# Kernel tuning notes

Measured on AMD Instinct MI355X. Metric: run time of the kernel, lower is better.

## Reference

```python
import jax, jax.numpy as jnp
import numpy as np

B, T, H, K, V, O = 4, 2048, 512, 128, 128, 512


def setup_inputs() -> dict:
    key = jax.random.key(0)
    k0, k1, k2 = jax.random.split(key, 3)
    hidden_state = jax.random.normal(k0, (B, T, H), dtype=jnp.float32)
    cell_state = jnp.zeros((B, K, V), dtype=jnp.float32)
    # fused projection: hidden -> [query K, key K, gate K, value V]
    lim_p = np.sqrt(6.0 / (H + 3 * K + V)).astype(np.float32)  # xavier uniform
    proj_w = jax.random.uniform(k1, (3 * K + V, H), jnp.float32, -lim_p, lim_p)
    proj_b = jnp.zeros((3 * K + V,), jnp.float32)
    lim_o = np.sqrt(6.0 / (2 * V + O)).astype(np.float32)
    out_w = jax.random.uniform(k2, (O, 2 * V), jnp.float32, -lim_o, lim_o)
    out_b = jnp.zeros((O,), jnp.float32)
    return {"hidden_state": hidden_state, "cell_state": cell_state,
            "proj_w": proj_w, "proj_b": proj_b, "out_w": out_w, "out_b": out_b}


def reference(hidden_state, cell_state, proj_w, proj_b, out_w, out_b):
    Bq, Tq, _ = hidden_state.shape
    qkgv = hidden_state @ proj_w.T + proj_b          # (B,T,3K+V)
    query = qkgv[..., :K]
    kgate = jax.nn.sigmoid(qkgv[..., K:2 * K])       # key (sigmoid)
    gate = jax.nn.sigmoid(qkgv[..., 2 * K:3 * K])
    value = jnp.tanh(qkgv[..., 3 * K:])              # (B,T,V)

    def step(C, xs):
        q_t, k_t, g_t, v_t = xs                      # (B,K),(B,K),(B,K),(B,V)
        C = C * g_t[..., None] + k_t[..., None] * v_t[..., None, :]  # (B,K,V)
        o_t = jnp.einsum('bkv,bk->bv', C, q_t)       # C^T q
        return C, o_t

    xs = (query.swapaxes(0, 1), kgate.swapaxes(0, 1),
          gate.swapaxes(0, 1), value.swapaxes(0, 1))
    C_final, ov = jax.lax.scan(step, cell_state, xs)
    ov = ov.swapaxes(0, 1)                           # (B,T,V) output_val per step

    # causal Luong dot attention over the growing bank of past output_vals
    scores = jnp.einsum('btv,bsv->bts', ov, ov)      # (B,T,T)
    causal = jnp.tril(jnp.ones((Tq, Tq), dtype=bool))
    scores = jnp.where(causal, scores, -jnp.inf)
    attn = jax.nn.softmax(scores, axis=-1)
    context = jnp.einsum('bts,bsv->btv', attn, ov)   # (B,T,V)

    outputs = jnp.concatenate([ov, context], axis=-1) @ out_w.T + out_b  # (B,T,O)
    return outputs, C_final
```

## Files before the change

### kernel.cpp

```cpp
#include <hip/hip_runtime.h>
#include <hip/hip_bf16.h>


typedef __attribute__((ext_vector_type(8))) short bf16x8;
typedef __attribute__((ext_vector_type(4))) float f32x4;
typedef __attribute__((ext_vector_type(4))) short short4v;

#define MFMA(a,b,c) __builtin_amdgcn_mfma_f32_16x16x32_bf16(a,b,c,0,0,0)

__device__ __forceinline__ short f2b(float x){
  union { float f; unsigned u; } v; v.f = x;
  unsigned r = v.u + 0x7fffu + ((v.u >> 16) & 1u);
  return (short)(r >> 16);
}
__device__ __forceinline__ float b2f(short h){
  union { unsigned u; float f; } v;
  v.u = ((unsigned)(unsigned short)h) << 16;
  return v.f;
}
__device__ __forceinline__ void split2(float x, short& h, short& l){
  h = f2b(x);
  l = f2b(x - b2f(h));
}
__device__ __forceinline__ void gload16(const void* g, void* l){
  __builtin_amdgcn_global_load_lds(
    (__attribute__((address_space(1))) unsigned int*)(void*)(g),
    (__attribute__((address_space(3))) unsigned int*)(l), 16, 0, 0);
}

__global__ void k_split(const float* __restrict__ in, short* __restrict__ hi,
                        short* __restrict__ lo, int n){
  int i = (blockIdx.x * blockDim.x + threadIdx.x) * 4;
  if (i < n){
    float4 v = *(const float4*)(in + i);
    short4v h, l;
    short th, tl;
    split2(v.x, th, tl); h.x = th; l.x = tl;
    split2(v.y, th, tl); h.y = th; l.y = tl;
    split2(v.z, th, tl); h.z = th; l.z = tl;
    split2(v.w, th, tl); h.w = th; l.w = tl;
    *(short4v*)(hi + i) = h;
    *(short4v*)(lo + i) = l;
  }
}

__global__ void k_cvt(const float* __restrict__ in, short* __restrict__ out, int n){
  int i = (blockIdx.x * blockDim.x + threadIdx.x) * 4;
  if (i < n){
    float4 v = *(const float4*)(in + i);
    short4v o; o.x = f2b(v.x); o.y = f2b(v.y); o.z = f2b(v.z); o.w = f2b(v.w);
    *(short4v*)(out + i) = o;
  }
}

__global__ __launch_bounds__(256) void k_gemm1(
    const short* __restrict__ Ah, const short* __restrict__ Al,
    const short* __restrict__ Bh, const short* __restrict__ Bl,
    const float* __restrict__ bias,
    float* __restrict__ q_o, float* __restrict__ kg_o,
    float* __restrict__ lg_o, float* __restrict__ vv_o)
{
  __shared__ __align__(16) short At[128*64];
  __shared__ __align__(16) short Bt[64*64];
  const int m0 = blockIdx.x * 128;
  const int ny = blockIdx.y;
  const int tid = threadIdx.x, lane = tid & 63;
  const int w = tid >> 6;
  const int wu = __builtin_amdgcn_readfirstlane(w);
  const int wr = w >> 1, wc = w & 1;
  const int coll = lane & 15, rq = lane >> 4;
  f32x4 acc[4][2];
#pragma unroll
  for (int i = 0; i < 4; i++)
#pragma unroll
    for (int j = 0; j < 2; j++) acc[i][j] = (f32x4){0.f,0.f,0.f,0.f};

  for (int step = 0; step < 24; ++step){
    const int seg = step >> 3;
    const int k0 = (step & 7) * 64;
    const short* Asrc = (seg < 2) ? Ah : Al;
    const short* Bsrc = (seg == 1) ? Bl : Bh;
    __syncthreads();
#pragma unroll
    for (int t = 0; t < 4; ++t){
      int ci0 = t*256 + wu*64;
      int ci = ci0 + lane;
      int row = ci >> 3;
      int cs = (ci & 7) ^ (row & 7);
      gload16(Asrc + (size_t)(m0 + row)*512 + k0 + cs*8, At + (size_t)ci0*8);
    }
#pragma unroll
    for (int t = 0; t < 2; ++t){
      int ci0 = t*256 + wu*64;
      int ci = ci0 + lane;
      int row = ci >> 3;
      int cs = (ci & 7) ^ (row & 7);
      gload16(Bsrc + (size_t)(ny*64 + row)*512 + k0 + cs*8, Bt + (size_t)ci0*8);
    }
    __syncthreads();
#pragma unroll
    for (int kk = 0; kk < 2; ++kk){
      bf16x8 a[4], b[2];
#pragma unroll
      for (int mi = 0; mi < 4; mi++){
        int ar = wr*64 + mi*16 + coll;
        a[mi] = *(const bf16x8*)&At[ar*64 + (((kk*4+rq) ^ (ar & 7))*8)];
      }
#pragma unroll
      for (int ni = 0; ni < 2; ni++){
        int br = wc*32 + ni*16 + coll;
        b[ni] = *(const bf16x8*)&Bt[br*64 + (((kk*4+rq) ^ (br & 7))*8)];
      }
#pragma unroll
      for (int mi = 0; mi < 4; mi++)
#pragma unroll
        for (int ni = 0; ni < 2; ni++)
          acc[mi][ni] = MFMA(a[mi], b[ni], acc[mi][ni]);
    }
  }
  const int sec = ny >> 1;
  const int jb  = (ny & 1) * 64;
#pragma unroll
  for (int mi = 0; mi < 4; mi++)
#pragma unroll
  for (int ni = 0; ni < 2; ni++){
    int gl = wc*32 + ni*16 + coll;
    float bsv = bias[ny*64 + gl];
    int jj = jb + gl;
#pragma unroll
    for (int r = 0; r < 4; r++){
      int gm = m0 + wr*64 + mi*16 + rq*4 + r;
      float v = acc[mi][ni][r] + bsv;
      size_t idx = (size_t)gm * 128 + jj;
      if (sec == 0)      q_o[idx] = v;
      else if (sec == 1) kg_o[idx] = 1.f / (1.f + __expf(-v));
      else if (sec == 2) lg_o[idx] = (v > 0.f) ? -log1pf(__expf(-v)) : (v - log1pf(__expf(v)));
      else               vv_o[idx] = tanhf(v);
    }
  }
}

__global__ __launch_bounds__(128) void k_prep(
  const float* __restrict__ q_f, const float* __restrict__ kg_f,
  const float* __restrict__ lg_f, const float* __restrict__ vv_f,
  short* __restrict__ qth, short* __restrict__ qtl,
  short* __restrict__ kth, short* __restrict__ ktl,
  short* __restrict__ khTh, short* __restrict__ khTl,
  short* __restrict__ vvTh, short* __restrict__ vvTl,
  float* __restrict__ Dend)
{
  const int bc = blockIdx.x;
  const int kx = threadIdx.x;
  const size_t base = ((size_t)(bc >> 6) * 2048 + (size_t)(bc & 63) * 32) * 128 + kx;
  double L[32];
  double Lr = 0.0;
#pragma unroll
  for (int s = 0; s < 32; s++){
    size_t idx = base + (size_t)s * 128;
    Lr += (double)lg_f[idx];
    L[s] = Lr;
    float lam  = __expf((float)Lr);
    float ilam = __expf((float)(-Lr));
    short h, l;
    split2(q_f[idx] * lam, h, l);  qth[idx] = h; qtl[idx] = l;
    split2(kg_f[idx] * ilam, h, l); kth[idx] = h; ktl[idx] = l;
  }
  const double Lend = Lr;
  Dend[(size_t)bc * 128 + kx] = (float)exp(Lend);
  __align__(16) short bufh[32], bufl[32];
#pragma unroll
  for (int s = 0; s < 32; s++){
    size_t idx = base + (size_t)s * 128;
    short h, l;
    split2(kg_f[idx] * __expf((float)(Lend - L[s])), h, l);
    bufh[s] = h; bufl[s] = l;
  }
  { short* dh = khTh + ((size_t)bc * 128 + kx) * 32;
    short* dl = khTl + ((size_t)bc * 128 + kx) * 32;
#pragma unroll
    for (int i = 0; i < 32; i += 8){
      *(bf16x8*)(dh + i) = *(const bf16x8*)(bufh + i);
      *(bf16x8*)(dl + i) = *(const bf16x8*)(bufl + i);
    } }
#pragma unroll
  for (int s = 0; s < 32; s++){
    short h, l;
    split2(vv_f[base + (size_t)s * 128], h, l);
    bufh[s] = h; bufl[s] = l;
  }
  { short* dh = vvTh + ((size_t)bc * 128 + kx) * 32;
    short* dl = vvTl + ((size_t)bc * 128 + kx) * 32;
#pragma unroll
    for (int i = 0; i < 32; i += 8){
      *(bf16x8*)(dh + i) = *(const bf16x8*)(bufh + i);
      *(bf16x8*)(dl + i) = *(const bf16x8*)(bufl + i);
    } }
}

__global__ __launch_bounds__(64) void k_scan(
  const short* __restrict__ khTh, const short* __restrict__ khTl,
  const short* __restrict__ vvTh, const short* __restrict__ vvTl,
  const float* __restrict__ Dend, const float* __restrict__ cell0,
  short* __restrict__ sth, short* __restrict__ stl, float* __restrict__ Cfin)
{
  const int blk = blockIdx.x;
  const int b = blk >> 6, tile = blk & 63;
  const int kt = tile >> 3, vt = tile & 7;
  const int lane = threadIdx.x & 63;
  const int coll = lane & 15, rq = lane >> 4;
  const int kcol = kt*16 + coll;
  const int vrow0 = vt*16 + rq*4;
  const size_t cb0 = (size_t)b * 64;

  f32x4 acc;
#pragma unroll
  for (int r = 0; r < 4; r++)
    acc[r] = cell0[((size_t)b*128 + kcol)*128 + vrow0 + r];

  size_t gv = (cb0*128 + vt*16 + coll)*32 + rq*8;
  size_t gk = (cb0*128 + kt*16 + coll)*32 + rq*8;
  bf16x8 avh = *(const bf16x8*)(vvTh + gv);
  bf16x8 avl = *(const bf16x8*)(vvTl + gv);
  bf16x8 bkh = *(const bf16x8*)(khTh + gk);
  bf16x8 bkl = *(const bf16x8*)(khTl + gk);
  float d = Dend[cb0*128 + kcol];

  for (int ck = 0; ck < 64; ck++){
    const size_t cb = cb0 + ck;
    const size_t cbn = cb0 + (ck < 63 ? ck + 1 : ck);
    size_t ngv = (cbn*128 + vt*16 + coll)*32 + rq*8;
    size_t ngk = (cbn*128 + kt*16 + coll)*32 + rq*8;
    bf16x8 navh = *(const bf16x8*)(vvTh + ngv);
    bf16x8 navl = *(const bf16x8*)(vvTl + ngv);
    bf16x8 nbkh = *(const bf16x8*)(khTh + ngk);
    bf16x8 nbkl = *(const bf16x8*)(khTl + ngk);
    float nd = Dend[cbn*128 + kcol];
    {
      size_t sb = (cb*128 + vrow0)*128 + kcol;
#pragma unroll
      for (int r = 0; r < 4; r++){
        short h, l; split2(acc[r], h, l);
        sth[sb + (size_t)r*128] = h;
        stl[sb + (size_t)r*128] = l;
      }
    }
#pragma unroll
    for (int r = 0; r < 4; r++) acc[r] *= d;
    acc = MFMA(avh, bkh, acc);
    acc = MFMA(avh, bkl, acc);
    acc = MFMA(avl, bkh, acc);
    avh = navh; avl = navl; bkh = nbkh; bkl = nbkl; d = nd;
  }
  *(f32x4*)(Cfin + ((size_t)b*128 + kcol)*128 + vrow0) = acc;
}

__global__ __launch_bounds__(256) void k_chunkout(
  const short* __restrict__ qth, const short* __restrict__ qtl,
  const short* __restrict__ kth, const short* __restrict__ ktl,
  const short* __restrict__ vvTh, const short* __restrict__ vvTl,
  const short* __restrict__ sth, const short* __restrict__ stl,
  short* __restrict__ ovT, short* __restrict__ ovc,
  short* __restrict__ ovqh, short* __restrict__ ovql)
{
  __shared__ __align__(16) short ATh[32][40], ATl[32][40];
  const int bc = blockIdx.x;
  const int b = bc >> 6, ck = bc & 63;
  const int tid = threadIdx.x, lane = tid & 63, w = tid >> 6;
  const int coll = lane & 15, rq = lane >> 4;
  const size_t tbase = (size_t)b * 2048 + (size_t)ck * 32;
  {
    const int si = w >> 1, ti = w & 1;
    f32x4 aA = (f32x4){0.f,0.f,0.f,0.f};
#pragma unroll
    for (int kit = 0; kit < 4; kit++){
      size_t ga = (tbase + si*16 + coll) * 128 + kit*32 + rq*8;
      size_t gb = (tbase + ti*16 + coll) * 128 + kit*32 + rq*8;
      bf16x8 a3h = *(const bf16x8*)(kth + ga), a3l = *(const bf16x8*)(ktl + ga);
      bf16x8 b3h = *(const bf16x8*)(qth + gb), b3l = *(const bf16x8*)(qtl + gb);
      aA = MFMA(a3h, b3h, aA);
      aA = MFMA(a3h, b3l, aA);
      aA = MFMA(a3l, b3h, aA);
    }
#pragma unroll
    for (int r = 0; r < 4; r++){
      int s = si*16 + rq*4 + r, t = ti*16 + coll;
      float val = (s <= t) ? aA[r] : 0.f;
      short h, l; split2(val, h, l);
      ATh[t][s] = h; ATl[t][s] = l;
    }
  }
  __syncthreads();
  const int vb = w * 32;
  f32x4 o[2][2];
#pragma unroll
  for (int vi = 0; vi < 2; vi++)
#pragma unroll
    for (int ti = 0; ti < 2; ti++) o[vi][ti] = (f32x4){0.f,0.f,0.f,0.f};
#pragma unroll
  for (int kit = 0; kit < 4; kit++){
    bf16x8 aCh[2], aCl[2], bqh[2], bql[2];
#pragma unroll
    for (int vi = 0; vi < 2; vi++){
      size_t g = ((size_t)bc * 128 + vb + vi*16 + coll) * 128 + kit*32 + rq*8;
      aCh[vi] = *(const bf16x8*)(sth + g);
      aCl[vi] = *(const bf16x8*)(stl + g);
    }
#pragma unroll
    for (int ti = 0; ti < 2; ti++){
      size_t g = (tbase + ti*16 + coll) * 128 + kit*32 + rq*8;
      bqh[ti] = *(const bf16x8*)(qth + g);
      bql[ti] = *(const bf16x8*)(qtl + g);
    }
#pragma unroll
    for (int vi = 0; vi < 2; vi++)
#pragma unroll
      for (int ti = 0; ti < 2; ti++){
        o[vi][ti] = MFMA(aCh[vi], bqh[ti], o[vi][ti]);
        o[vi][ti] = MFMA(aCh[vi], bql[ti], o[vi][ti]);
        o[vi][ti] = MFMA(aCl[vi], bqh[ti], o[vi][ti]);
      }
  }
  {
    bf16x8 a2h[2], a2l[2], b2h[2], b2l[2];
#pragma unroll
    for (int vi = 0; vi < 2; vi++){
      size_t g = ((size_t)bc * 128 + vb + vi*16 + coll) * 32 + rq*8;
      a2h[vi] = *(const bf16x8*)(vvTh + g);
      a2l[vi] = *(const bf16x8*)(vvTl + g);
    }
#pragma unroll
    for (int ti = 0; ti < 2; ti++){
      b2h[ti] = *(const bf16x8*)&ATh[ti*16 + coll][rq*8];
      b2l[ti] = *(const bf16x8*)&ATl[ti*16 + coll][rq*8];
    }
#pragma unroll
    for (int vi = 0; vi < 2; vi++)
#pragma unroll
      for (int ti = 0; ti < 2; ti++){
        o[vi][ti] = MFMA(a2h[vi], b2h[ti], o[vi][ti]);
        o[vi][ti] = MFMA(a2h[vi], b2l[ti], o[vi][ti]);
        o[vi][ti] = MFMA(a2l[vi], b2h[ti], o[vi][ti]);
      }
  }
#pragma unroll
  for (int vi = 0; vi < 2; vi++)
#pragma unroll
  for (int ti = 0; ti < 2; ti++)
#pragma unroll
  for (int r = 0; r < 4; r++){
    int v = vb + vi*16 + rq*4 + r;
    int tl = ti*16 + coll;
    float val = o[vi][ti][r];
    short h, l; split2(val, h, l);
    ovT[((size_t)b * 128 + v) * 2048 + (size_t)ck * 32 + tl] = h;
    ovc[(tbase + tl) * 256 + v] = h;
    ovqh[(tbase + tl) * 128 + v] = h;
    ovql[(tbase + tl) * 128 + v] = l;
  }
}

__global__ __launch_bounds__(256) void k_attn(
  const short* __restrict__ ovqh, const short* __restrict__ ovql,
  const short* __restrict__ ovT,
  float* __restrict__ m_part, float* __restrict__ l_part,
  short* __restrict__ oa_part)
{
  const int qi = blockIdx.x, b = blockIdx.y, p = blockIdx.z;
  const int qbase = qi * 64;
  const int ps = p * 256;
  const size_t obase = (size_t)b * 2048;
  const int tid = threadIdx.x;
  if (ps > qbase + 63){
    if (tid < 64) l_part[((obase + qbase + tid) << 3) + p] = 0.f;
    return;
  }
  __shared__ __align__(16) short P[4][16][40];
  const int lane = tid & 63, w = tid >> 6;
  const int coll = lane & 15, rq = lane >> 4;
  const int tw = qbase + w * 16;
  bf16x8 qfh[4], qfl[4];
#pragma unroll
  for (int kit = 0; kit < 4; kit++){
    size_t g = (obase + tw + coll) * 128 + kit*32 + rq*8;
    qfh[kit] = *(const bf16x8*)(ovqh + g);
    qfl[kit] = *(const bf16x8*)(ovql + g);
  }
  float m[4], l[4];
  f32x4 oa[8];
#pragma unroll
  for (int r = 0; r < 4; r++){ m[r] = -1e30f; l[r] = 0.f; }
#pragma unroll
  for (int df = 0; df < 8; df++) oa[df] = (f32x4){0.f,0.f,0.f,0.f};
  const int send = min(tw + 15, ps + 255);
  for (int s0 = ps; s0 <= send; s0 += 32){
    f32x4 sc[2];
#pragma unroll
    for (int sf = 0; sf < 2; sf++){
      bf16x8 kh[4], kl[4];
#pragma unroll
      for (int kit = 0; kit < 4; kit++){
        size_t g = (obase + s0 + sf*16 + coll) * 128 + kit*32 + rq*8;
        kh[kit] = *(const bf16x8*)(ovqh + g);
        kl[kit] = *(const bf16x8*)(ovql + g);
      }
      f32x4 c0 = (f32x4){0.f,0.f,0.f,0.f};
      f32x4 c1 = (f32x4){0.f,0.f,0.f,0.f};
      f32x4 c2 = (f32x4){0.f,0.f,0.f,0.f};
#pragma unroll
      for (int kit = 0; kit < 4; kit++){
        c0 = MFMA(qfh[kit], kh[kit], c0);
        c1 = MFMA(qfh[kit], kl[kit], c1);
        c2 = MFMA(qfl[kit], kh[kit], c2);
      }
      sc[sf] = c0 + c1 + c2;
    }
    bf16x8 vf[8];
#pragma unroll
    for (int df = 0; df < 8; df++)
      vf[df] = *(const bf16x8*)(ovT + ((size_t)b*128 + df*16 + coll)*2048 + s0 + rq*8);
#pragma unroll
    for (int r = 0; r < 4; r++){
      int trow = tw + rq*4 + r;
      float s0v = (s0 + coll      <= trow) ? sc[0][r] : -1e30f;
      float s1v = (s0 + 16 + coll <= trow) ? sc[1][r] : -1e30f;
      float mx = fmaxf(s0v, s1v);
#pragma unroll
      for (int d = 1; d < 16; d <<= 1) mx = fmaxf(mx, __shfl_xor(mx, d));
      float mn = fmaxf(m[r], mx);
      float scale = __expf(m[r] - mn);
      float p0 = __expf(s0v - mn);
      float p1 = __expf(s1v - mn);
      float rs = p0 + p1;
#pragma unroll
      for (int d = 1; d < 16; d <<= 1) rs += __shfl_xor(rs, d);
      l[r] = l[r] * scale + rs;
      m[r] = mn;
#pragma unroll
      for (int df = 0; df < 8; df++) oa[df][r] *= scale;
      P[w][rq*4 + r][coll]      = f2b(p0);
      P[w][rq*4 + r][16 + coll] = f2b(p1);
    }
    bf16x8 pf = *(const bf16x8*)&P[w][coll][rq*8];
#pragma unroll
    for (int df = 0; df < 8; df++)
      oa[df] = MFMA(pf, vf[df], oa[df]);
  }
#pragma unroll
  for (int r = 0; r < 4; r++){
    int t = tw + rq*4 + r;
    size_t idx8 = ((obase + t) << 3) + p;
    if (coll == 0){ m_part[idx8] = m[r]; l_part[idx8] = l[r]; }
#pragma unroll
    for (int df = 0; df < 8; df++)
      oa_part[idx8*128 + df*16 + coll] = f2b(oa[df][r]);
  }
}

__global__ __launch_bounds__(256) void k_comb(
  const float* __restrict__ m_part, const float* __restrict__ l_part,
  const short* __restrict__ oa_part, short* __restrict__ ovc)
{
  const int blk = blockIdx.x;
  const int b = blk >> 5, qi = blk & 31;
  const int row = threadIdx.x >> 2, cg = threadIdx.x & 3;
  const int t = qi*64 + row;
  const size_t base8 = ((size_t)b*2048 + t) * 8;
  float mv[8], lv[8];
#pragma unroll
  for (int p = 0; p < 8; p++){ mv[p] = m_part[base8+p]; lv[p] = l_part[base8+p]; }
  float M = -3e38f;
#pragma unroll
  for (int p = 0; p < 8; p++) if (lv[p] > 0.f) M = fmaxf(M, mv[p]);
  float L = 0.f, wgt[8];
#pragma unroll
  for (int p = 0; p < 8; p++){
    wgt[p] = (lv[p] > 0.f) ? __expf(mv[p] - M) : 0.f;
    L += lv[p] * wgt[p];
  }
  const float inv = 1.f / L;
  const int v0 = cg * 32;
  float acc[32];
#pragma unroll
  for (int j = 0; j < 32; j++) acc[j] = 0.f;
#pragma unroll
  for (int p = 0; p < 8; p++){
    if (lv[p] > 0.f){
      const short* src = oa_part + (base8 + p)*128 + v0;
#pragma unroll
      for (int jo = 0; jo < 32; jo += 8){
        bf16x8 x = *(const bf16x8*)(src + jo);
#pragma unroll
        for (int j = 0; j < 8; j++) acc[jo+j] += b2f(x[j]) * wgt[p];
      }
    }
  }
  short* dst = ovc + ((size_t)b*2048 + t)*256 + 128 + v0;
#pragma unroll
  for (int jo = 0; jo < 32; jo += 8){
    bf16x8 o;
#pragma unroll
    for (int j = 0; j < 8; j++) o[j] = f2b(acc[jo+j] * inv);
    *(bf16x8*)(dst + jo) = o;
  }
}

__global__ __launch_bounds__(256) void k_gemm0(
  const short* __restrict__ A, const short* __restrict__ Bw,
  const float* __restrict__ bias, float* __restrict__ out)
{
  __shared__ __align__(16) short At[128*64];
  __shared__ __align__(16) short Bt[64*64];
  const int m0 = blockIdx.x * 128;
  const int ny = blockIdx.y;
  const int tid = threadIdx.x, lane = tid & 63;
  const int w = tid >> 6;
  const int wu = __builtin_amdgcn_readfirstlane(w);
  const int wr = w >> 1, wc = w & 1;
  const int coll = lane & 15, rq = lane >> 4;
  f32x4 acc[4][2];
#pragma unroll
  for (int i = 0; i < 4; i++)
#pragma unroll
    for (int j = 0; j < 2; j++) acc[i][j] = (f32x4){0.f,0.f,0.f,0.f};

  for (int step = 0; step < 4; ++step){
    const int k0 = step * 64;
    __syncthreads();
#pragma unroll
    for (int t = 0; t < 4; ++t){
      int ci0 = t*256 + wu*64;
      int ci = ci0 + lane;
      int row = ci >> 3;
      int cs = (ci & 7) ^ (row & 7);
      gload16(A + (size_t)(m0 + row)*256 + k0 + cs*8, At + (size_t)ci0*8);
    }
#pragma unroll
    for (int t = 0; t < 2; ++t){
      int ci0 = t*256 + wu*64;
      int ci = ci0 + lane;
      int row = ci >> 3;
      int cs = (ci & 7) ^ (row & 7);
      gload16(Bw + (size_t)(ny*64 + row)*256 + k0 + cs*8, Bt + (size_t)ci0*8);
    }
    __syncthreads();
#pragma unroll
    for (int kk = 0; kk < 2; ++kk){
      bf16x8 a[4], b[2];
#pragma unroll
      for (int mi = 0; mi < 4; mi++){
        int ar = wr*64 + mi*16 + coll;
        a[mi] = *(const bf16x8*)&At[ar*64 + (((kk*4+rq) ^ (ar & 7))*8)];
      }
#pragma unroll
      for (int ni = 0; ni < 2; ni++){
        int br = wc*32 + ni*16 + coll;
        b[ni] = *(const bf16x8*)&Bt[br*64 + (((kk*4+rq) ^ (br & 7))*8)];
      }
#pragma unroll
      for (int mi = 0; mi < 4; mi++)
#pragma unroll
        for (int ni = 0; ni < 2; ni++)
          acc[mi][ni] = MFMA(a[mi], b[ni], acc[mi][ni]);
    }
  }
#pragma unroll
  for (int mi = 0; mi < 4; mi++)
#pragma unroll
  for (int ni = 0; ni < 2; ni++){
    int gn = ny*64 + wc*32 + ni*16 + coll;
    float bsv = bias[gn];
#pragma unroll
    for (int r = 0; r < 4; r++){
      int gm = m0 + wr*64 + mi*16 + rq*4 + r;
      out[(size_t)gm * 512 + gn] = acc[mi][ni][r] + bsv;
    }
  }
}

extern "C" void kernel_launch(void* const* d_in, const int* in_sizes, int n_in,
                              void* d_out, int out_size, void* d_ws, size_t ws_size,
                              hipStream_t stream){
  const float* hidden = (const float*)d_in[0];
  const float* cell0  = (const float*)d_in[1];
  const float* projw  = (const float*)d_in[2];
  const float* projb  = (const float*)d_in[3];
  const float* outw   = (const float*)d_in[4];
  const float* outb   = (const float*)d_in[5];
  float* out = (float*)d_out;

  char* ws = (char*)d_ws;
  size_t off = 0;
  auto alloc = [&](size_t bytes) -> void* {
    void* p = ws + off;
    off += (bytes + 255) & ~(size_t)255;
    return p;
  };
  short* Xh   = (short*)alloc(8192ULL * 512 * 2);
  short* Xl   = (short*)alloc(8192ULL * 512 * 2);
  short* ovqh = Xh;
  short* ovql = Xh + 1048576;
  short* ovT  = Xh + 2097152;
  short* ovc  = Xh + 3145728;
  float* q_f  = (float*)alloc(8192ULL * 128 * 4);
  float* kg_f = (float*)alloc(8192ULL * 128 * 4);
  float* lg_f = (float*)alloc(8192ULL * 128 * 4);
  float* vv_f = (float*)alloc(8192ULL * 128 * 4);
  short* sth  = (short*)q_f;
  short* stl  = sth + 4194304;
  short* oa_part = (short*)q_f;
  short* Wh   = (short*)alloc(512ULL * 512 * 2);
  short* Wl   = (short*)alloc(512ULL * 512 * 2);
  short* OWbf = (short*)alloc(512ULL * 256 * 2);
  short* qth  = (short*)alloc(8192ULL * 128 * 2);
  short* qtl  = (short*)alloc(8192ULL * 128 * 2);
  short* kth  = (short*)alloc(8192ULL * 128 * 2);
  short* ktl  = (short*)alloc(8192ULL * 128 * 2);
  short* khTh = (short*)alloc(256ULL * 128 * 32 * 2);
  short* khTl = (short*)alloc(256ULL * 128 * 32 * 2);
  short* vvTh = (short*)alloc(256ULL * 128 * 32 * 2);
  short* vvTl = (short*)alloc(256ULL * 128 * 32 * 2);
  float* Dend = (float*)alloc(256ULL * 128 * 4);
  float* m_part = (float*)alloc(4ULL * 2048 * 8 * 4);
  float* l_part = (float*)alloc(4ULL * 2048 * 8 * 4);

  k_split<<<4096, 256, 0, stream>>>(hidden, Xh, Xl, 8192 * 512);
  k_split<<<256,  256, 0, stream>>>(projw,  Wh, Wl, 512 * 512);
  k_cvt<<<128, 256, 0, stream>>>(outw, OWbf, 512 * 256);

  k_gemm1<<<dim3(64, 8), 256, 0, stream>>>(Xh, Xl, Wh, Wl, projb, q_f, kg_f, lg_f, vv_f);
  k_prep<<<256, 128, 0, stream>>>(q_f, kg_f, lg_f, vv_f,
                                  qth, qtl, kth, ktl, khTh, khTl, vvTh, vvTl, Dend);
  k_scan<<<256, 64, 0, stream>>>(khTh, khTl, vvTh, vvTl, Dend, cell0,
                                 sth, stl, out + 8192ULL * 512);
  k_chunkout<<<256, 256, 0, stream>>>(qth, qtl, kth, ktl, vvTh, vvTl, sth, stl,
                                      ovT, ovc, ovqh, ovql);
  k_attn<<<dim3(32, 4, 8), 256, 0, stream>>>(ovqh, ovql, ovT, m_part, l_part, oa_part);
  k_comb<<<128, 256, 0, stream>>>(m_part, l_part, oa_part, ovc);
  k_gemm0<<<dim3(64, 8), 256, 0, stream>>>(ovc, OWbf, outb, out);
}
```

Before: 294.1 us.

## Fuse split-bf16 passes and widen N tile in projection GEMM

The projection GEMM used to stream the hi/lo split operands as three separate K passes of 64-wide tiles. It now loads Ah, Al, Bh and Bl together once per K step and issues the three MFMA products (hh, hl, lh) from the same LDS data. The N tile grows from 64 to 128, which halves the grid to 64x4 blocks. Global and LDS loads per MFMA go down, at the cost of 64KB of LDS per block, double the accumulator registers, and only 256 blocks, so occupancy drops.

```diff
diff --git a/kernel.cpp b/kernel.cpp
--- a/kernel.cpp
+++ b/kernel.cpp
@@ -60,8 +60,7 @@
     float* __restrict__ q_o, float* __restrict__ kg_o,
     float* __restrict__ lg_o, float* __restrict__ vv_o)
 {
-  __shared__ __align__(16) short At[128*64];
-  __shared__ __align__(16) short Bt[64*64];
+  __shared__ __align__(16) short AhT[128*64], AlT[128*64], BhT[128*64], BlT[128*64];
   const int m0 = blockIdx.x * 128;
   const int ny = blockIdx.y;
   const int tid = threadIdx.x, lane = tid & 63;
@@ -69,17 +68,14 @@
   const int wu = __builtin_amdgcn_readfirstlane(w);
   const int wr = w >> 1, wc = w & 1;
   const int coll = lane & 15, rq = lane >> 4;
-  f32x4 acc[4][2];
+  f32x4 acc[4][4];
 #pragma unroll
   for (int i = 0; i < 4; i++)
 #pragma unroll
-    for (int j = 0; j < 2; j++) acc[i][j] = (f32x4){0.f,0.f,0.f,0.f};
-
-  for (int step = 0; step < 24; ++step){
-    const int seg = step >> 3;
-    const int k0 = (step & 7) * 64;
-    const short* Asrc = (seg < 2) ? Ah : Al;
-    const short* Bsrc = (seg == 1) ? Bl : Bh;
+    for (int j = 0; j < 4; j++) acc[i][j] = (f32x4){0.f,0.f,0.f,0.f};
+
+  for (int step = 0; step < 8; ++step){
+    const int k0 = step * 64;
     __syncthreads();
 #pragma unroll
     for (int t = 0; t < 4; ++t){
@@ -87,51 +83,53 @@
       int ci = ci0 + lane;
       int row = ci >> 3;
       int cs = (ci & 7) ^ (row & 7);
-      gload16(Asrc + (size_t)(m0 + row)*512 + k0 + cs*8, At + (size_t)ci0*8);
-    }
-#pragma unroll
-    for (int t = 0; t < 2; ++t){
-      int ci0 = t*256 + wu*64;
-      int ci = ci0 + lane;
-      int row = ci >> 3;
-      int cs = (ci & 7) ^ (row & 7);
-      gload16(Bsrc + (size_t)(ny*64 + row)*512 + k0 + cs*8, Bt + (size_t)ci0*8);
+      size_t ga = (size_t)(m0 + row)*512 + k0 + cs*8;
+      size_t gb = (size_t)(ny*128 + row)*512 + k0 + cs*8;
+      gload16(Ah + ga, AhT + (size_t)ci0*8);
+      gload16(Al + ga, AlT + (size_t)ci0*8);
+      gload16(Bh + gb, BhT + (size_t)ci0*8);
+      gload16(Bl + gb, BlT + (size_t)ci0*8);
     }
     __syncthreads();
 #pragma unroll
     for (int kk = 0; kk < 2; ++kk){
-      bf16x8 a[4], b[2];
+      bf16x8 ah[4], al[4], bh[4], bl[4];
 #pragma unroll
       for (int mi = 0; mi < 4; mi++){
         int ar = wr*64 + mi*16 + coll;
-        a[mi] = *(const bf16x8*)&At[ar*64 + (((kk*4+rq) ^ (ar & 7))*8)];
-      }
-#pragma unroll
-      for (int ni = 0; ni < 2; ni++){
-        int br = wc*32 + ni*16 + coll;
-        b[ni] = *(const bf16x8*)&Bt[br*64 + (((kk*4+rq) ^ (br & 7))*8)];
+        int off = ar*64 + (((kk*4+rq) ^ (ar & 7))*8);
+        ah[mi] = *(const bf16x8*)&AhT[off];
+        al[mi] = *(const bf16x8*)&AlT[off];
+      }
+#pragma unroll
+      for (int ni = 0; ni < 4; ni++){
+        int br = wc*64 + ni*16 + coll;
+        int off = br*64 + (((kk*4+rq) ^ (br & 7))*8);
+        bh[ni] = *(const bf16x8*)&BhT[off];
+        bl[ni] = *(const bf16x8*)&BlT[off];
       }
 #pragma unroll
       for (int mi = 0; mi < 4; mi++)
 #pragma unroll
-        for (int ni = 0; ni < 2; ni++)
-          acc[mi][ni] = MFMA(a[mi], b[ni], acc[mi][ni]);
-    }
-  }
-  const int sec = ny >> 1;
-  const int jb  = (ny & 1) * 64;
+        for (int ni = 0; ni < 4; ni++){
+          acc[mi][ni] = MFMA(ah[mi], bh[ni], acc[mi][ni]);
+          acc[mi][ni] = MFMA(ah[mi], bl[ni], acc[mi][ni]);
+          acc[mi][ni] = MFMA(al[mi], bh[ni], acc[mi][ni]);
+        }
+    }
+  }
+  const int sec = ny;
 #pragma unroll
   for (int mi = 0; mi < 4; mi++)
 #pragma unroll
-  for (int ni = 0; ni < 2; ni++){
-    int gl = wc*32 + ni*16 + coll;
-    float bsv = bias[ny*64 + gl];
-    int jj = jb + gl;
+  for (int ni = 0; ni < 4; ni++){
+    int gl = wc*64 + ni*16 + coll;
+    float bsv = bias[ny*128 + gl];
 #pragma unroll
     for (int r = 0; r < 4; r++){
       int gm = m0 + wr*64 + mi*16 + rq*4 + r;
       float v = acc[mi][ni][r] + bsv;
-      size_t idx = (size_t)gm * 128 + jj;
+      size_t idx = (size_t)gm * 128 + gl;
       if (sec == 0)      q_o[idx] = v;
       else if (sec == 1) kg_o[idx] = 1.f / (1.f + __expf(-v));
       else if (sec == 2) lg_o[idx] = (v > 0.f) ? -log1pf(__expf(-v)) : (v - log1pf(__expf(v)));
@@ -627,7 +625,7 @@
   k_split<<<256,  256, 0, stream>>>(projw,  Wh, Wl, 512 * 512);
   k_cvt<<<128, 256, 0, stream>>>(outw, OWbf, 512 * 256);
 
-  k_gemm1<<<dim3(64, 8), 256, 0, stream>>>(Xh, Xl, Wh, Wl, projb, q_f, kg_f, lg_f, vv_f);
+  k_gemm1<<<dim3(64, 4), 256, 0, stream>>>(Xh, Xl, Wh, Wl, projb, q_f, kg_f, lg_f, vv_f);
   k_prep<<<256, 128, 0, stream>>>(q_f, kg_f, lg_f, vv_f,
                                   qth, qtl, kth, ktl, khTh, khTl, vvTh, vvTl, Dend);
   k_scan<<<256, 64, 0, stream>>>(khTh, khTl, vvTh, vvTl, Dend, cell0,
```

After: 366.8 us. 1.25x slower.
